# Performance work log

Hardware: AMD Instinct MI355X
Metric: run time of the kernel (lower is better)

Reference implementation:

```python
import jax, jax.numpy as jnp
import numpy as np

N_WAY = 64
EPS = 1e-5  # torch LayerNorm default


def _layernorm(x, g, b):
    mu = jnp.mean(x, axis=-1, keepdims=True)
    var = jnp.mean(jnp.square(x - mu), axis=-1, keepdims=True)
    return (x - mu) * jax.lax.rsqrt(var + EPS) * g + b


def _backbone(x, params):
    (W1, b1, g1, be1, W2, b2, g2, be2, W3, b3, g3, be3, W4, b4) = params
    h = jax.nn.relu(_layernorm(x @ W1.T + b1, g1, be1))
    h = jax.nn.relu(_layernorm(h @ W2.T + b2, g2, be2))
    h = jax.nn.relu(_layernorm(h @ W3.T + b3, g3, be3))
    return h @ W4.T + b4


def setup_inputs() -> dict:
    key = jax.random.key(0)
    ks = jax.random.split(key, 20)
    d = {}
    d["support_features"] = jax.random.normal(ks[0], (32768, 768), jnp.float32)
    d["support_labels"] = jax.random.randint(ks[1], (32768,), 0, N_WAY, jnp.int64)
    d["query_features"] = jax.random.normal(ks[2], (65536, 768), jnp.float32)
    dims = [(512, 768), (512, 512), (128, 512), (32, 128)]
    ki = 3
    for i, (dout, din) in enumerate(dims, start=1):
        scale = 1.0 / np.sqrt(din)
        d[f"W{i}"] = jax.random.uniform(ks[ki], (dout, din), jnp.float32, -scale, scale); ki += 1
        d[f"b{i}"] = jax.random.uniform(ks[ki], (dout,), jnp.float32, -scale, scale); ki += 1
        if i < 4:
            d[f"g{i}"] = jnp.ones((dout,), jnp.float32)
            d[f"be{i}"] = jnp.zeros((dout,), jnp.float32)
    return d


def reference(support_features, support_labels, query_features,
              W1, b1, g1, be1, W2, b2, g2, be2, W3, b3, g3, be3, W4, b4):
    params = (W1, b1, g1, be1, W2, b2, g2, be2, W3, b3, g3, be3, W4, b4)
    z_support = _backbone(support_features, params)   # [Ns, 32]
    z_query = _backbone(query_features, params)       # [Nq, 32]
    # segment-mean prototypes (replaces per-class nonzero+mean loop)
    sums = jax.ops.segment_sum(z_support, support_labels, num_segments=N_WAY)
    counts = jax.ops.segment_sum(jnp.ones((z_support.shape[0],), z_support.dtype),
                                 support_labels, num_segments=N_WAY)
    z_proto = sums / jnp.maximum(counts, 1.0)[:, None]  # [n_way, 32]
    # -cdist (euclidean)
    sq = (jnp.sum(z_query * z_query, axis=1)[:, None]
          + jnp.sum(z_proto * z_proto, axis=1)[None, :]
          - 2.0 * z_query @ z_proto.T)
    return -jnp.sqrt(jnp.maximum(sq, 0.0))  # [Nq, n_way]
```

## Files before the change

kernel.cpp:

```cpp
#include <hip/hip_runtime.h>

typedef unsigned short u16;
typedef short bf16x8 __attribute__((ext_vector_type(8)));
typedef float f32x16 __attribute__((ext_vector_type(16)));
typedef unsigned short u16x4v __attribute__((ext_vector_type(4)));
typedef unsigned short u16x8v __attribute__((ext_vector_type(8)));

#define LN_EPS 1e-5f

__device__ __forceinline__ u16 f2bf(float v) {
    unsigned x = __float_as_uint(v);
    x += 0x7fffu + ((x >> 16) & 1u);
    return (u16)(x >> 16);
}
__device__ __forceinline__ float bf2f(u16 u) {
    return __uint_as_float(((unsigned)u) << 16);
}

#define GLD16(gp, lp) __builtin_amdgcn_global_load_lds( \
    (const __attribute__((address_space(1))) void*)(gp), \
    (__attribute__((address_space(3))) void*)(lp), 16, 0, 0)

__global__ __launch_bounds__(256)
void swizzle_split(const float* __restrict__ src, u16* __restrict__ hi,
                   u16* __restrict__ lo, int R, int DIN)
{
    __shared__ __align__(16) u16 SH[2][24][17][8];
    const int tid  = threadIdx.x;
    const int row0 = blockIdx.x * 16;
    const int QK   = DIN / 16;
    const int kq0  = QK * blockIdx.y;
    const int NKC  = DIN / 32;

    const int slots = 16 * QK;
    for (int s = tid; s < slots; s += 256) {
        int row = s / QK, kq = s % QK;
        float4 v = *(const float4*)(src + (long)(row0 + row) * DIN + (long)(kq0 + kq) * 4);
        int kc = kq >> 1, jh = (kq & 1) * 4;
        float vv[4] = {v.x, v.y, v.z, v.w};
        u16x4v h, l;
#pragma unroll
        for (int j = 0; j < 4; ++j) {
            u16 hb = f2bf(vv[j]);
            h[j] = hb;
            l[j] = f2bf(vv[j] - bf2f(hb));
        }
        *(u16x4v*)(&SH[0][kc][row][jh]) = h;
        *(u16x4v*)(&SH[1][kc][row][jh]) = l;
    }
    __syncthreads();
    const int chunks = NKC * 16;
    for (int s = tid; s < chunks; s += 256) {
        int row = s & 15, kc = s >> 4;
        long o = ((long)(kq0 / 2 + kc) * R + row0 + row) * 8;
        *(u16x8v*)(hi + o) = *(const u16x8v*)(&SH[0][kc][row][0]);
        *(u16x8v*)(lo + o) = *(const u16x8v*)(&SH[1][kc][row][0]);
    }
}

template<int DOUT, int OUT_MODE, int NT>
__device__ __forceinline__ void ln_epilogue(
    f32x16 (&acc)[2][NT], float (&lnp)[4][64][2],
    const float* __restrict__ bias, const float* __restrict__ gam,
    const float* __restrict__ bet,
    u16* __restrict__ Yh, u16* __restrict__ Yl, float* __restrict__ Yf,
    float* __restrict__ Hlds,
    long row0, int NR, int wv, int l31, int hh)
{
    float gg[NT], bb[NT], bev[NT];
#pragma unroll
    for (int u = 0; u < NT; ++u) {
        int c = wv * (DOUT / 4) + u * 32 + l31;
        bb[u] = bias[c]; gg[u] = gam[c]; bev[u] = bet[c];
    }
#pragma unroll
    for (int t = 0; t < 2; ++t)
#pragma unroll
        for (int r = 0; r < 16; ++r) {
            float s1 = 0.f, s2 = 0.f;
#pragma unroll
            for (int u = 0; u < NT; ++u) {
                float v = acc[t][u][r] + bb[u];
                acc[t][u][r] = v;
                s1 += v; s2 += v * v;
            }
#pragma unroll
            for (int off = 1; off < 32; off <<= 1) {
                s1 += __shfl_xor(s1, off, 64);
                s2 += __shfl_xor(s2, off, 64);
            }
            int row = t * 32 + (r & 3) + 8 * (r >> 2) + 4 * hh;
            if (l31 == r) { lnp[wv][row][0] = s1; lnp[wv][row][1] = s2; }
        }
    __syncthreads();
#pragma unroll
    for (int t = 0; t < 2; ++t)
#pragma unroll
        for (int r = 0; r < 16; ++r) {
            int row = t * 32 + (r & 3) + 8 * (r >> 2) + 4 * hh;
            float s1 = lnp[0][row][0] + lnp[1][row][0] + lnp[2][row][0] + lnp[3][row][0];
            float s2 = lnp[0][row][1] + lnp[1][row][1] + lnp[2][row][1] + lnp[3][row][1];
            float mean = s1 * (1.f / DOUT);
            float inv  = rsqrtf(s2 * (1.f / DOUT) - mean * mean + LN_EPS);
            long gr = row0 + row;
#pragma unroll
            for (int u = 0; u < NT; ++u) {
                int c = wv * (DOUT / 4) + u * 32 + l31;
                float v = (acc[t][u][r] - mean) * inv * gg[u] + bev[u];
                v = fmaxf(v, 0.f);
                if constexpr (OUT_MODE == 1) {
                    u16 hv = f2bf(v);
                    long o = ((long)(c >> 3) * NR + gr) * 8 + (c & 7);
                    Yh[o] = hv;
                    Yl[o] = f2bf(v - bf2f(hv));
                } else if constexpr (OUT_MODE == 2) {
                    Hlds[row * 129 + c] = v;
                } else {
                    Yf[gr * DOUT + c] = v;
                }
            }
        }
}

template<int NT>
__device__ __forceinline__ void mfma_step(
    const u16*& wph, const u16*& wpl, long wstep,
    const u16* AL0, const u16* AL1,
    f32x16 (&acc)[2][NT], int l31)
{
    bf16x8 wf[NT][2], af[2][2];
#pragma unroll
    for (int u = 0; u < NT; ++u) {
        wf[u][0] = *(const bf16x8*)(wph + u * 256);
        wf[u][1] = *(const bf16x8*)(wpl + u * 256);
    }
    wph += wstep; wpl += wstep;
#pragma unroll
    for (int t = 0; t < 2; ++t) {
        af[t][0] = *(const bf16x8*)(AL0 + (t * 32 + l31) * 8);
        af[t][1] = *(const bf16x8*)(AL1 + (t * 32 + l31) * 8);
    }
#pragma unroll
    for (int t = 0; t < 2; ++t)
#pragma unroll
        for (int u = 0; u < NT; ++u)
            acc[t][u] = __builtin_amdgcn_mfma_f32_32x32x16_bf16(af[t][0], wf[u][0], acc[t][u], 0, 0, 0);
#pragma unroll
    for (int t = 0; t < 2; ++t)
#pragma unroll
        for (int u = 0; u < NT; ++u)
            acc[t][u] = __builtin_amdgcn_mfma_f32_32x32x16_bf16(af[t][0], wf[u][1], acc[t][u], 0, 0, 0);
#pragma unroll
    for (int t = 0; t < 2; ++t)
#pragma unroll
        for (int u = 0; u < NT; ++u)
            acc[t][u] = __builtin_amdgcn_mfma_f32_32x32x16_bf16(af[t][1], wf[u][0], acc[t][u], 0, 0, 0);
}

template<int DOUT>
__global__ __launch_bounds__(256, 2)
void mfma_layer1(const float* __restrict__ X,
                 const u16* __restrict__ Wh, const u16* __restrict__ Wl,
                 const float* __restrict__ bias, const float* __restrict__ gam,
                 const float* __restrict__ bet,
                 u16* __restrict__ Yh, u16* __restrict__ Yl,
                 int DIN, int NR, long rbase)
{
    constexpr int NT = DOUT / 128;
    __shared__ __align__(16) u16 AL[2][4][2][2][520];
    __shared__ float lnp[4][64][2];

    const int tid  = threadIdx.x;
    const int lane = tid & 63, wv = tid >> 6;
    const int l31  = lane & 31, hh = lane >> 5;
    const long lrow0 = (long)blockIdx.x * 64;
    const long row0  = rbase + lrow0;

    const int srow  = wv * 16 + (lane >> 2);
    const int kpart = lane & 3;
    const float* xp = X + (lrow0 + srow) * DIN + kpart * 16;

    const u16* wph = Wh + ((long)hh * DOUT + wv * (DOUT / 4) + l31) * 8;
    const u16* wpl = Wl + ((long)hh * DOUT + wv * (DOUT / 4) + l31) * 8;
    const long wstep = (long)2 * DOUT * 8;

    f32x16 acc[2][NT];
#pragma unroll
    for (int t = 0; t < 2; ++t)
#pragma unroll
        for (int u = 0; u < NT; ++u)
#pragma unroll
            for (int e = 0; e < 16; ++e) acc[t][u][e] = 0.f;

    const int nslab = DIN / 64;

    auto stage = [&](const float* p, int buf) {
#pragma unroll
        for (int c = 0; c < 2; ++c) {
            float4 v0 = *(const float4*)(p + c * 8);
            float4 v1 = *(const float4*)(p + c * 8 + 4);
            float f[8] = {v0.x, v0.y, v0.z, v0.w, v1.x, v1.y, v1.z, v1.w};
            u16x8v h, l;
#pragma unroll
            for (int j = 0; j < 8; ++j) {
                u16 hb = f2bf(f[j]);
                h[j] = hb;
                l[j] = f2bf(f[j] - bf2f(hb));
            }
            *(u16x8v*)(&AL[buf][kpart][0][c][srow * 8]) = h;
            *(u16x8v*)(&AL[buf][kpart][1][c][srow * 8]) = l;
        }
    };

    stage(xp, 0);
    for (int sl = 0; sl < nslab; ++sl) {
        __syncthreads();
        const int cb = sl & 1;
        if (sl + 1 < nslab) stage(xp + (sl + 1) * 64, cb ^ 1);
#pragma unroll
        for (int s = 0; s < 4; ++s) {
            mfma_step<NT>(wph, wpl, wstep,
                          &AL[cb][s][0][hh][0], &AL[cb][s][1][hh][0],
                          acc, l31);
        }
    }

    ln_epilogue<DOUT, 1, NT>(acc, lnp, bias, gam, bet, Yh, Yl, nullptr, nullptr,
                             row0, NR, wv, l31, hh);
}

template<int DOUT, int OUT_MODE>
__global__ __launch_bounds__(256, 2)
void mfma_layer(const u16* __restrict__ Ah, const u16* __restrict__ Al,
                const u16* __restrict__ Wh, const u16* __restrict__ Wl,
                const float* __restrict__ bias, const float* __restrict__ gam,
                const float* __restrict__ bet,
                u16* __restrict__ Yh, u16* __restrict__ Yl,
                float* __restrict__ Yf, int DIN, int NR,
                const float* __restrict__ W4, const float* __restrict__ b4)
{
    constexpr int NT = DOUT / 128;
    __shared__ __align__(16) u16 AL[2][4][2][2][64 * 8];
    __shared__ float lnp[4][64][2];
    __shared__ float Hs[OUT_MODE == 2 ? 64 * 129 : 1];

    const int tid  = threadIdx.x;
    const int lane = tid & 63, wv = tid >> 6;
    const int l31  = lane & 31, hh = lane >> 5;
    const long row0 = (long)blockIdx.x * 64;

    const u16* gpA[4];
    const long stA = (long)8 * NR * 8;
#pragma unroll
    for (int t = 0; t < 4; ++t) {
        int p = t & 1, c = t >> 1;
        const u16* base = p ? Al : Ah;
        gpA[t] = base + ((long)(2 * wv + c) * NR + row0 + lane) * 8;
    }

    const u16* wph = Wh + ((long)hh * DOUT + wv * (DOUT / 4) + l31) * 8;
    const u16* wpl = Wl + ((long)hh * DOUT + wv * (DOUT / 4) + l31) * 8;
    const long wstep = (long)2 * DOUT * 8;

    f32x16 acc[2][NT];
#pragma unroll
    for (int t = 0; t < 2; ++t)
#pragma unroll
        for (int u = 0; u < NT; ++u)
#pragma unroll
            for (int e = 0; e < 16; ++e) acc[t][u][e] = 0.f;

    const int nslab = DIN / 64;
#pragma unroll
    for (int t = 0; t < 4; ++t) {
        GLD16(gpA[t], &AL[0][wv][t & 1][t >> 1][0]);
        gpA[t] += stA;
    }

    for (int sl = 0; sl < nslab; ++sl) {
        __syncthreads();
        const int cb = sl & 1;
        if (sl + 1 < nslab) {
#pragma unroll
            for (int t = 0; t < 4; ++t) {
                GLD16(gpA[t], &AL[cb ^ 1][wv][t & 1][t >> 1][0]);
                gpA[t] += stA;
            }
        }
#pragma unroll
        for (int s = 0; s < 4; ++s) {
            mfma_step<NT>(wph, wpl, wstep,
                          &AL[cb][s][0][hh][0], &AL[cb][s][1][hh][0],
                          acc, l31);
        }
    }

    ln_epilogue<DOUT, OUT_MODE, NT>(acc, lnp, bias, gam, bet, Yh, Yl, Yf, Hs,
                                    row0, NR, wv, l31, hh);

    if constexpr (OUT_MODE == 2) {
        __syncthreads();
        const int rowl = tid & 63;
        const int og   = wv;
        float a4[8];
#pragma unroll
        for (int j = 0; j < 8; ++j) a4[j] = 0.f;
        for (int k = 0; k < 128; k += 4) {
            float h0 = Hs[rowl * 129 + k + 0];
            float h1 = Hs[rowl * 129 + k + 1];
            float h2 = Hs[rowl * 129 + k + 2];
            float h3 = Hs[rowl * 129 + k + 3];
#pragma unroll
            for (int j = 0; j < 8; ++j) {
                const float4 w = *(const float4*)(W4 + (og * 8 + j) * 128 + k);
                a4[j] = fmaf(h0, w.x, fmaf(h1, w.y, fmaf(h2, w.z, fmaf(h3, w.w, a4[j]))));
            }
        }
        const long gr = row0 + rowl;
#pragma unroll
        for (int j = 0; j < 8; ++j) Yf[gr * 32 + og * 8 + j] = a4[j] + b4[og * 8 + j];
    }
}

__global__ __launch_bounds__(256)
void proto_k(const float* __restrict__ Zs, const int* __restrict__ lab,
             float* __restrict__ P)
{
    const int c = blockIdx.x;
    const int tid = threadIdx.x, lane = tid & 63, wv = tid >> 6;
    float acc[32];
#pragma unroll
    for (int d = 0; d < 32; ++d) acc[d] = 0.f;
    float cnt = 0.f;
    for (int i = tid; i < 32768; i += 256) {
        if (lab[i] == c) {
            cnt += 1.f;
#pragma unroll
            for (int d = 0; d < 32; ++d) acc[d] += Zs[(long)i * 32 + d];
        }
    }
    __shared__ float wsum[4][32];
    __shared__ float wcnt[4];
#pragma unroll
    for (int d = 0; d < 32; ++d) {
        float v = acc[d];
        for (int off = 32; off > 0; off >>= 1) v += __shfl_xor(v, off, 64);
        if (lane == 0) wsum[wv][d] = v;
    }
    {
        float v = cnt;
        for (int off = 32; off > 0; off >>= 1) v += __shfl_xor(v, off, 64);
        if (lane == 0) wcnt[wv] = v;
    }
    __syncthreads();
    if (tid < 32) {
        float s  = wsum[0][tid] + wsum[1][tid] + wsum[2][tid] + wsum[3][tid];
        float cn = wcnt[0] + wcnt[1] + wcnt[2] + wcnt[3];
        P[c * 32 + tid] = s / fmaxf(cn, 1.f);
    }
}

__global__ __launch_bounds__(256)
void dist_k(const float* __restrict__ Zq, const float* __restrict__ P,
            float* __restrict__ O)
{
    __shared__ float ps[64 * 32];
    __shared__ float pn[64];
    const int tid = threadIdx.x;
    for (int idx = tid; idx < 2048; idx += 256) ps[idx] = P[idx];
    __syncthreads();
    if (tid < 64) {
        float s = 0.f;
        for (int d = 0; d < 32; ++d) { float v = ps[tid * 32 + d]; s += v * v; }
        pn[tid] = s;
    }
    __syncthreads();

    long q = (long)blockIdx.x * 256 + tid;
    float zr[32];
#pragma unroll
    for (int d = 0; d < 32; d += 4) {
        float4 v = *(const float4*)(Zq + q * 32 + d);
        zr[d] = v.x; zr[d + 1] = v.y; zr[d + 2] = v.z; zr[d + 3] = v.w;
    }
    float zz = 0.f;
#pragma unroll
    for (int d = 0; d < 32; ++d) zz += zr[d] * zr[d];
    for (int p = 0; p < 64; ++p) {
        float dot = 0.f;
#pragma unroll
        for (int d = 0; d < 32; ++d) dot = fmaf(zr[d], ps[p * 32 + d], dot);
        float sq = zz + pn[p] - 2.f * dot;
        O[q * 64 + p] = -sqrtf(fmaxf(sq, 0.f));
    }
}

extern "C" void kernel_launch(void* const* d_in, const int* in_sizes, int n_in,
                              void* d_out, int out_size, void* d_ws, size_t ws_size,
                              hipStream_t stream)
{
    const float* supp = (const float*)d_in[0];
    const int*   lab  = (const int*)  d_in[1];
    const float* qry  = (const float*)d_in[2];
    const float* W1 = (const float*)d_in[3];  const float* b1 = (const float*)d_in[4];
    const float* g1 = (const float*)d_in[5];  const float* be1= (const float*)d_in[6];
    const float* W2 = (const float*)d_in[7];  const float* b2 = (const float*)d_in[8];
    const float* g2 = (const float*)d_in[9];  const float* be2= (const float*)d_in[10];
    const float* W3 = (const float*)d_in[11]; const float* b3 = (const float*)d_in[12];
    const float* g3 = (const float*)d_in[13]; const float* be3= (const float*)d_in[14];
    const float* W4 = (const float*)d_in[15]; const float* b4 = (const float*)d_in[16];
    float* out = (float*)d_out;

    const long NTOT = 98304, NS = 32768, NQ = 65536;
    const int  NR = (int)NTOT;

    char* wsp = (char*)d_ws;
    size_t off = 0;
    auto take = [&](size_t bytes) {
        char* p = wsp + off;
        off += (bytes + 255) & ~(size_t)255;
        return (void*)p;
    };

    float* zAll  = (float*)take((size_t)NTOT * 32 * 4);
    float* proto = (float*)take(2048 * 4);
    u16* W1h = (u16*)take((size_t)512 * 768 * 2);
    u16* W1l = (u16*)take((size_t)512 * 768 * 2);
    u16* W2h = (u16*)take((size_t)512 * 512 * 2);
    u16* W2l = (u16*)take((size_t)512 * 512 * 2);
    u16* W3h = (u16*)take((size_t)128 * 512 * 2);
    u16* W3l = (u16*)take((size_t)128 * 512 * 2);
    u16* h1h = (u16*)take((size_t)NTOT * 512 * 2);
    u16* h1l = (u16*)take((size_t)NTOT * 512 * 2);
    u16* h2h = (u16*)take((size_t)NTOT * 512 * 2);
    u16* h2l = (u16*)take((size_t)NTOT * 512 * 2);

    swizzle_split<<<dim3(32, 4), dim3(256), 0, stream>>>(W1, W1h, W1l, 512, 768);
    swizzle_split<<<dim3(32, 4), dim3(256), 0, stream>>>(W2, W2h, W2l, 512, 512);
    swizzle_split<<<dim3(8, 4),  dim3(256), 0, stream>>>(W3, W3h, W3l, 128, 512);

    mfma_layer1<512><<<dim3(NS / 64), dim3(256), 0, stream>>>(
        supp, W1h, W1l, b1, g1, be1, h1h, h1l, 768, NR, 0);
    mfma_layer1<512><<<dim3(NQ / 64), dim3(256), 0, stream>>>(
        qry, W1h, W1l, b1, g1, be1, h1h, h1l, 768, NR, NS);

    mfma_layer<512, 1><<<dim3(NTOT / 64), dim3(256), 0, stream>>>(
        h1h, h1l, W2h, W2l, b2, g2, be2, h2h, h2l, nullptr, 512, NR,
        nullptr, nullptr);
    mfma_layer<128, 2><<<dim3(NTOT / 64), dim3(256), 0, stream>>>(
        h2h, h2l, W3h, W3l, b3, g3, be3, nullptr, nullptr, zAll, 512, NR,
        W4, b4);

    proto_k<<<dim3(64),  dim3(256), 0, stream>>>(zAll, lab, proto);
    dist_k<<<dim3(256), dim3(256), 0, stream>>>(zAll + NS * 32, proto, out);
}
```

Before: 1.013 ms.

## Halve row tile to 32 for layers 1-2 and alias layer-3 LDS buffers

Layers 1 and 2 now process 32 rows per block instead of 64. This halves the accumulator registers and LDS per block, and the launch bound is raised to 3 blocks per SM. Layer 3 reuses the A-tile LDS buffer for the post-LayerNorm activations instead of a separate 33KB array, which lets it request 4 blocks per SM. The aim is higher occupancy and better latency hiding, at the cost of reloading each weight fragment for half as many rows, which doubles weight traffic per output row.

```diff
diff --git a/kernel.cpp b/kernel.cpp
--- a/kernel.cpp
+++ b/kernel.cpp
@@ -58,9 +58,9 @@
     }
 }
 
-template<int DOUT, int OUT_MODE, int NT>
+template<int DOUT, int OUT_MODE, int NT, int TROWS>
 __device__ __forceinline__ void ln_epilogue(
-    f32x16 (&acc)[2][NT], float (&lnp)[4][64][2],
+    f32x16 (&acc)[TROWS][NT], float (&lnp)[4][TROWS * 32][2],
     const float* __restrict__ bias, const float* __restrict__ gam,
     const float* __restrict__ bet,
     u16* __restrict__ Yh, u16* __restrict__ Yl, float* __restrict__ Yf,
@@ -74,7 +74,7 @@
         bb[u] = bias[c]; gg[u] = gam[c]; bev[u] = bet[c];
     }
 #pragma unroll
-    for (int t = 0; t < 2; ++t)
+    for (int t = 0; t < TROWS; ++t)
 #pragma unroll
         for (int r = 0; r < 16; ++r) {
             float s1 = 0.f, s2 = 0.f;
@@ -94,7 +94,7 @@
         }
     __syncthreads();
 #pragma unroll
-    for (int t = 0; t < 2; ++t)
+    for (int t = 0; t < TROWS; ++t)
 #pragma unroll
         for (int r = 0; r < 16; ++r) {
             int row = t * 32 + (r & 3) + 8 * (r >> 2) + 4 * hh;
@@ -122,13 +122,13 @@
         }
 }
 
-template<int NT>
+template<int NT, int TROWS>
 __device__ __forceinline__ void mfma_step(
     const u16*& wph, const u16*& wpl, long wstep,
     const u16* AL0, const u16* AL1,
-    f32x16 (&acc)[2][NT], int l31)
-{
-    bf16x8 wf[NT][2], af[2][2];
+    f32x16 (&acc)[TROWS][NT], int l31)
+{
+    bf16x8 wf[NT][2], af[TROWS][2];
 #pragma unroll
     for (int u = 0; u < NT; ++u) {
         wf[u][0] = *(const bf16x8*)(wph + u * 256);
@@ -136,80 +136,75 @@
     }
     wph += wstep; wpl += wstep;
 #pragma unroll
-    for (int t = 0; t < 2; ++t) {
+    for (int t = 0; t < TROWS; ++t) {
         af[t][0] = *(const bf16x8*)(AL0 + (t * 32 + l31) * 8);
         af[t][1] = *(const bf16x8*)(AL1 + (t * 32 + l31) * 8);
     }
 #pragma unroll
-    for (int t = 0; t < 2; ++t)
+    for (int t = 0; t < TROWS; ++t)
 #pragma unroll
         for (int u = 0; u < NT; ++u)
             acc[t][u] = __builtin_amdgcn_mfma_f32_32x32x16_bf16(af[t][0], wf[u][0], acc[t][u], 0, 0, 0);
 #pragma unroll
-    for (int t = 0; t < 2; ++t)
+    for (int t = 0; t < TROWS; ++t)
 #pragma unroll
         for (int u = 0; u < NT; ++u)
             acc[t][u] = __builtin_amdgcn_mfma_f32_32x32x16_bf16(af[t][0], wf[u][1], acc[t][u], 0, 0, 0);
 #pragma unroll
-    for (int t = 0; t < 2; ++t)
+    for (int t = 0; t < TROWS; ++t)
 #pragma unroll
         for (int u = 0; u < NT; ++u)
             acc[t][u] = __builtin_amdgcn_mfma_f32_32x32x16_bf16(af[t][1], wf[u][0], acc[t][u], 0, 0, 0);
 }
 
 template<int DOUT>
-__global__ __launch_bounds__(256, 2)
-void mfma_layer1(const float* __restrict__ X,
-                 const u16* __restrict__ Wh, const u16* __restrict__ Wl,
-                 const float* __restrict__ bias, const float* __restrict__ gam,
-                 const float* __restrict__ bet,
-                 u16* __restrict__ Yh, u16* __restrict__ Yl,
-                 int DIN, int NR, long rbase)
+__global__ __launch_bounds__(256, 3)
+void mfma_layer1_r32(const float* __restrict__ X,
+                     const u16* __restrict__ Wh, const u16* __restrict__ Wl,
+                     const float* __restrict__ bias, const float* __restrict__ gam,
+                     const float* __restrict__ bet,
+                     u16* __restrict__ Yh, u16* __restrict__ Yl,
+                     int DIN, int NR, long rbase)
 {
     constexpr int NT = DOUT / 128;
-    __shared__ __align__(16) u16 AL[2][4][2][2][520];
-    __shared__ float lnp[4][64][2];
+    __shared__ __align__(16) u16 AL[2][4][2][2][264];
+    __shared__ float lnp[4][32][2];
 
     const int tid  = threadIdx.x;
     const int lane = tid & 63, wv = tid >> 6;
     const int l31  = lane & 31, hh = lane >> 5;
-    const long lrow0 = (long)blockIdx.x * 64;
+    const long lrow0 = (long)blockIdx.x * 32;
     const long row0  = rbase + lrow0;
 
-    const int srow  = wv * 16 + (lane >> 2);
-    const int kpart = lane & 3;
-    const float* xp = X + (lrow0 + srow) * DIN + kpart * 16;
+    const int srow  = tid >> 3;
+    const int kpart = tid & 7;
+    const float* xp = X + (lrow0 + srow) * DIN + kpart * 8;
 
     const u16* wph = Wh + ((long)hh * DOUT + wv * (DOUT / 4) + l31) * 8;
     const u16* wpl = Wl + ((long)hh * DOUT + wv * (DOUT / 4) + l31) * 8;
     const long wstep = (long)2 * DOUT * 8;
 
-    f32x16 acc[2][NT];
-#pragma unroll
-    for (int t = 0; t < 2; ++t)
-#pragma unroll
-        for (int u = 0; u < NT; ++u)
-#pragma unroll
-            for (int e = 0; e < 16; ++e) acc[t][u][e] = 0.f;
+    f32x16 acc[1][NT];
+#pragma unroll
+    for (int u = 0; u < NT; ++u)
+#pragma unroll
+        for (int e = 0; e < 16; ++e) acc[0][u][e] = 0.f;
 
     const int nslab = DIN / 64;
 
     auto stage = [&](const float* p, int buf) {
-#pragma unroll
-        for (int c = 0; c < 2; ++c) {
-            float4 v0 = *(const float4*)(p + c * 8);
-            float4 v1 = *(const float4*)(p + c * 8 + 4);
-            float f[8] = {v0.x, v0.y, v0.z, v0.w, v1.x, v1.y, v1.z, v1.w};
-            u16x8v h, l;
-#pragma unroll
-            for (int j = 0; j < 8; ++j) {
-                u16 hb = f2bf(f[j]);
-                h[j] = hb;
-                l[j] = f2bf(f[j] - bf2f(hb));
-            }
-            *(u16x8v*)(&AL[buf][kpart][0][c][srow * 8]) = h;
-            *(u16x8v*)(&AL[buf][kpart][1][c][srow * 8]) = l;
-        }
+        float4 v0 = *(const float4*)(p);
+        float4 v1 = *(const float4*)(p + 4);
+        float f[8] = {v0.x, v0.y, v0.z, v0.w, v1.x, v1.y, v1.z, v1.w};
+        u16x8v h, l;
+#pragma unroll
+        for (int j = 0; j < 8; ++j) {
+            u16 hb = f2bf(f[j]);
+            h[j] = hb;
+            l[j] = f2bf(f[j] - bf2f(hb));
+        }
+        *(u16x8v*)(&AL[buf][kpart >> 1][0][kpart & 1][srow * 8]) = h;
+        *(u16x8v*)(&AL[buf][kpart >> 1][1][kpart & 1][srow * 8]) = l;
     };
 
     stage(xp, 0);
@@ -219,30 +214,94 @@
         if (sl + 1 < nslab) stage(xp + (sl + 1) * 64, cb ^ 1);
 #pragma unroll
         for (int s = 0; s < 4; ++s) {
-            mfma_step<NT>(wph, wpl, wstep,
-                          &AL[cb][s][0][hh][0], &AL[cb][s][1][hh][0],
-                          acc, l31);
-        }
-    }
-
-    ln_epilogue<DOUT, 1, NT>(acc, lnp, bias, gam, bet, Yh, Yl, nullptr, nullptr,
-                             row0, NR, wv, l31, hh);
-}
-
-template<int DOUT, int OUT_MODE>
-__global__ __launch_bounds__(256, 2)
-void mfma_layer(const u16* __restrict__ Ah, const u16* __restrict__ Al,
-                const u16* __restrict__ Wh, const u16* __restrict__ Wl,
-                const float* __restrict__ bias, const float* __restrict__ gam,
-                const float* __restrict__ bet,
-                u16* __restrict__ Yh, u16* __restrict__ Yl,
-                float* __restrict__ Yf, int DIN, int NR,
-                const float* __restrict__ W4, const float* __restrict__ b4)
+            mfma_step<NT, 1>(wph, wpl, wstep,
+                             &AL[cb][s][0][hh][0], &AL[cb][s][1][hh][0],
+                             acc, l31);
+        }
+    }
+
+    ln_epilogue<DOUT, 1, NT, 1>(acc, lnp, bias, gam, bet, Yh, Yl, nullptr,
+                                nullptr, row0, NR, wv, l31, hh);
+}
+
+template<int DOUT>
+__global__ __launch_bounds__(256, 3)
+void mfma_layer_r32(const u16* __restrict__ Ah, const u16* __restrict__ Al,
+                    const u16* __restrict__ Wh, const u16* __restrict__ Wl,
+                    const float* __restrict__ bias, const float* __restrict__ gam,
+                    const float* __restrict__ bet,
+                    u16* __restrict__ Yh, u16* __restrict__ Yl,
+                    int DIN, int NR)
 {
     constexpr int NT = DOUT / 128;
-    __shared__ __align__(16) u16 AL[2][4][2][2][64 * 8];
+    __shared__ __align__(16) u16 AL[2][4][2][2][256];
+    __shared__ float lnp[4][32][2];
+
+    const int tid  = threadIdx.x;
+    const int lane = tid & 63, wv = tid >> 6;
+    const int l31  = lane & 31, hh = lane >> 5;
+    const long row0 = (long)blockIdx.x * 32;
+
+    const u16* gp[2];
+#pragma unroll
+    for (int i = 0; i < 2; ++i) {
+        const u16* base = i ? Al : Ah;
+        gp[i] = base + ((long)(2 * wv + hh) * NR + row0 + l31) * 8;
+    }
+    const long stA = (long)8 * NR * 8;
+
+    const u16* wph = Wh + ((long)hh * DOUT + wv * (DOUT / 4) + l31) * 8;
+    const u16* wpl = Wl + ((long)hh * DOUT + wv * (DOUT / 4) + l31) * 8;
+    const long wstep = (long)2 * DOUT * 8;
+
+    f32x16 acc[1][NT];
+#pragma unroll
+    for (int u = 0; u < NT; ++u)
+#pragma unroll
+        for (int e = 0; e < 16; ++e) acc[0][u][e] = 0.f;
+
+    const int nslab = DIN / 64;
+#pragma unroll
+    for (int i = 0; i < 2; ++i) {
+        GLD16(gp[i], &AL[0][wv][i][0][0]);
+        gp[i] += stA;
+    }
+
+    for (int sl = 0; sl < nslab; ++sl) {
+        __syncthreads();
+        const int cb = sl & 1;
+        if (sl + 1 < nslab) {
+#pragma unroll
+            for (int i = 0; i < 2; ++i) {
+                GLD16(gp[i], &AL[cb ^ 1][wv][i][0][0]);
+                gp[i] += stA;
+            }
+        }
+#pragma unroll
+        for (int s = 0; s < 4; ++s) {
+            mfma_step<NT, 1>(wph, wpl, wstep,
+                             &AL[cb][s][0][hh][0], &AL[cb][s][1][hh][0],
+                             acc, l31);
+        }
+    }
+
+    ln_epilogue<DOUT, 1, NT, 1>(acc, lnp, bias, gam, bet, Yh, Yl, nullptr,
+                                nullptr, row0, NR, wv, l31, hh);
+}
+
+template<int DOUT>
+__global__ __launch_bounds__(256, 4)
+void mfma_layer3(const u16* __restrict__ Ah, const u16* __restrict__ Al,
+                 const u16* __restrict__ Wh, const u16* __restrict__ Wl,
+                 const float* __restrict__ bias, const float* __restrict__ gam,
+                 const float* __restrict__ bet,
+                 float* __restrict__ Yf, int DIN, int NR,
+                 const float* __restrict__ W4, const float* __restrict__ b4)
+{
+    constexpr int NT = DOUT / 128;
+    __shared__ __align__(16) u16 AL[2][4][2][2][520];
     __shared__ float lnp[4][64][2];
-    __shared__ float Hs[OUT_MODE == 2 ? 64 * 129 : 1];
+    float* Hs = (float*)&AL[0][0][0][0][0];
 
     const int tid  = threadIdx.x;
     const int lane = tid & 63, wv = tid >> 6;
@@ -289,37 +348,35 @@
         }
 #pragma unroll
         for (int s = 0; s < 4; ++s) {
-            mfma_step<NT>(wph, wpl, wstep,
-                          &AL[cb][s][0][hh][0], &AL[cb][s][1][hh][0],
-                          acc, l31);
-        }
-    }
-
-    ln_epilogue<DOUT, OUT_MODE, NT>(acc, lnp, bias, gam, bet, Yh, Yl, Yf, Hs,
-                                    row0, NR, wv, l31, hh);
-
-    if constexpr (OUT_MODE == 2) {
-        __syncthreads();
-        const int rowl = tid & 63;
-        const int og   = wv;
-        float a4[8];
-#pragma unroll
-        for (int j = 0; j < 8; ++j) a4[j] = 0.f;
-        for (int k = 0; k < 128; k += 4) {
-            float h0 = Hs[rowl * 129 + k + 0];
-            float h1 = Hs[rowl * 129 + k + 1];
-            float h2 = Hs[rowl * 129 + k + 2];
-            float h3 = Hs[rowl * 129 + k + 3];
-#pragma unroll
-            for (int j = 0; j < 8; ++j) {
-                const float4 w = *(const float4*)(W4 + (og * 8 + j) * 128 + k);
-                a4[j] = fmaf(h0, w.x, fmaf(h1, w.y, fmaf(h2, w.z, fmaf(h3, w.w, a4[j]))));
-            }
-        }
-        const long gr = row0 + rowl;
-#pragma unroll
-        for (int j = 0; j < 8; ++j) Yf[gr * 32 + og * 8 + j] = a4[j] + b4[og * 8 + j];
-    }
+            mfma_step<NT, 2>(wph, wpl, wstep,
+                             &AL[cb][s][0][hh][0], &AL[cb][s][1][hh][0],
+                             acc, l31);
+        }
+    }
+
+    ln_epilogue<DOUT, 2, NT, 2>(acc, lnp, bias, gam, bet, nullptr, nullptr,
+                                Yf, Hs, row0, NR, wv, l31, hh);
+
+    __syncthreads();
+    const int rowl = tid & 63;
+    const int og   = wv;
+    float a4[8];
+#pragma unroll
+    for (int j = 0; j < 8; ++j) a4[j] = 0.f;
+    for (int k = 0; k < 128; k += 4) {
+        float h0 = Hs[rowl * 129 + k + 0];
+        float h1 = Hs[rowl * 129 + k + 1];
+        float h2 = Hs[rowl * 129 + k + 2];
+        float h3 = Hs[rowl * 129 + k + 3];
+#pragma unroll
+        for (int j = 0; j < 8; ++j) {
+            const float4 w = *(const float4*)(W4 + (og * 8 + j) * 128 + k);
+            a4[j] = fmaf(h0, w.x, fmaf(h1, w.y, fmaf(h2, w.z, fmaf(h3, w.w, a4[j]))));
+        }
+    }
+    const long gr = row0 + rowl;
+#pragma unroll
+    for (int j = 0; j < 8; ++j) Yf[gr * 32 + og * 8 + j] = a4[j] + b4[og * 8 + j];
 }
 
 __global__ __launch_bounds__(256)
@@ -439,17 +496,15 @@
     swizzle_split<<<dim3(32, 4), dim3(256), 0, stream>>>(W2, W2h, W2l, 512, 512);
     swizzle_split<<<dim3(8, 4),  dim3(256), 0, stream>>>(W3, W3h, W3l, 128, 512);
 
-    mfma_layer1<512><<<dim3(NS / 64), dim3(256), 0, stream>>>(
+    mfma_layer1_r32<512><<<dim3(NS / 32), dim3(256), 0, stream>>>(
         supp, W1h, W1l, b1, g1, be1, h1h, h1l, 768, NR, 0);
-    mfma_layer1<512><<<dim3(NQ / 64), dim3(256), 0, stream>>>(
+    mfma_layer1_r32<512><<<dim3(NQ / 32), dim3(256), 0, stream>>>(
         qry, W1h, W1l, b1, g1, be1, h1h, h1l, 768, NR, NS);
 
-    mfma_layer<512, 1><<<dim3(NTOT / 64), dim3(256), 0, stream>>>(
-        h1h, h1l, W2h, W2l, b2, g2, be2, h2h, h2l, nullptr, 512, NR,
-        nullptr, nullptr);
-    mfma_layer<128, 2><<<dim3(NTOT / 64), dim3(256), 0, stream>>>(
-        h2h, h2l, W3h, W3l, b3, g3, be3, nullptr, nullptr, zAll, 512, NR,
-        W4, b4);
+    mfma_layer_r32<512><<<dim3(NTOT / 32), dim3(256), 0, stream>>>(
+        h1h, h1l, W2h, W2l, b2, g2, be2, h2h, h2l, 512, NR);
+    mfma_layer3<128><<<dim3(NTOT / 64), dim3(256), 0, stream>>>(
+        h2h, h2l, W3h, W3l, b3, g3, be3, zAll, 512, NR, W4, b4);
 
     proto_k<<<dim3(64),  dim3(256), 0, stream>>>(zAll, lab, proto);
     dist_k<<<dim3(256), dim3(256), 0, stream>>>(zAll + NS * 32, proto, out);
```

After: 1.080 ms. +6.6%, slower.
